# Kernel optimization log

Measured on AMD Instinct MI355X. Metric: run time of the kernel, lower is better.

The kernel has to match this reference:

```python
import jax, jax.numpy as jnp
import numpy as np

EPS = 1e-5

def _act_quant(x, bits=8):
    # per-token absmax quantization to signed int range, dequantized (STE)
    qb = float(2 ** (bits - 1) - 1)  # 127 for 8 bits
    scale = qb / jnp.clip(jnp.max(jnp.abs(x), axis=-1, keepdims=True), EPS, None)
    x_dq = jnp.clip(jnp.round(x * scale), -qb, qb) / scale
    return x + jax.lax.stop_gradient(x_dq - x)

def _weight_quant(w):
    # BitNet b1.58 ternary weights: scale = mean |W|, values in {-1,0,1} * scale (STE)
    s = jnp.clip(jnp.mean(jnp.abs(w)), EPS, None)
    w_dq = jnp.clip(jnp.round(w / s), -1.0, 1.0) * s
    return w + jax.lax.stop_gradient(w_dq - w)

def _bitlinear(x, w, bits=8):
    # x: [..., in], w: [out, in]
    return jnp.einsum('bsi,oi->bso', _act_quant(x, bits), _weight_quant(w))

def setup_inputs() -> dict:
    key = jax.random.key(0)
    k1, k2, k3 = jax.random.split(key, 3)
    B, S, H = 4, 4096, 2048
    I = int(H * 2.0)
    return {
        'hidden_states': jax.random.normal(k1, (B, S, H), dtype=jnp.float32),
        'w_up': jax.random.normal(k2, (I, H), dtype=jnp.float32) * (1.0 / np.sqrt(H)),
        'w_down': jax.random.normal(k3, (H, I), dtype=jnp.float32) * (1.0 / np.sqrt(I)),
    }

def reference(hidden_states, w_up, w_down):
    bits = 8
    h = _bitlinear(hidden_states, w_up, bits)          # [B,S,I]
    h = jnp.square(jax.nn.relu(h))                      # squared ReLU
    # dropout p=0.0 (eval) -> identity
    out = _bitlinear(h, w_down, bits)                   # [B,S,H]
    return out
```

## Files before the change

### kernel.cpp

```cpp
#include <hip/hip_runtime.h>
#include <hip/hip_bf16.h>

typedef unsigned short u16;
typedef signed char i8_t;
typedef _Float16 half_t;
typedef float v4fl __attribute__((ext_vector_type(4)));
typedef _Float16 v8h __attribute__((ext_vector_type(8)));
typedef int v4i __attribute__((ext_vector_type(4)));
typedef signed char v8c __attribute__((ext_vector_type(8)));
typedef signed char v16c __attribute__((ext_vector_type(16)));

#define BM 128
#define BN 128
#define BK 64

__device__ __forceinline__ float ternqf(float w, float s) {
    float q = rintf(w / s);
    return fminf(1.f, fmaxf(-1.f, q));
}

__device__ __forceinline__ void gload16(const void* g, void* l) {
    __builtin_amdgcn_global_load_lds(
        (const __attribute__((address_space(1))) void*)g,
        (__attribute__((address_space(3))) void*)l, 16, 0, 0);
}

__global__ void abssum_partial(const float* __restrict__ w, long n,
                               float* __restrict__ partial) {
    long i0 = ((long)blockIdx.x * 256 + threadIdx.x) * 8;
    long stride = (long)gridDim.x * 256 * 8;
    float s = 0.f;
    for (long i = i0; i < n; i += stride) {
        v4fl a = *(const v4fl*)(w + i);
        v4fl b = *(const v4fl*)(w + i + 4);
#pragma unroll
        for (int j = 0; j < 4; ++j) s += fabsf(a[j]) + fabsf(b[j]);
    }
#pragma unroll
    for (int off = 32; off > 0; off >>= 1) s += __shfl_down(s, off, 64);
    __shared__ __align__(16) float red[4];
    if ((threadIdx.x & 63) == 0) red[threadIdx.x >> 6] = s;
    __syncthreads();
    if (threadIdx.x == 0)
        partial[blockIdx.x] = (red[0] + red[1]) + (red[2] + red[3]);
}

__global__ void abssum_final(const float* __restrict__ part_up,
                             const float* __restrict__ part_dn,
                             float* __restrict__ scales, float inv) {
    const int wv = threadIdx.x >> 6;
    const int l = threadIdx.x & 63;
    const float* part = wv ? part_dn : part_up;
    float s = ((part[l] + part[l + 64]) + (part[l + 128] + part[l + 192]));
#pragma unroll
    for (int off = 32; off > 0; off >>= 1) s += __shfl_down(s, off, 64);
    if (l == 0) scales[wv] = fmaxf(s * inv, 1e-5f);
}

__global__ void wquant_kernel(const float* __restrict__ w, i8_t* __restrict__ wq,
                              const float* __restrict__ scale) {
    float s = scale[0];
    long i = ((long)blockIdx.x * 256 + threadIdx.x) * 8;
    v4fl a = *(const v4fl*)(w + i);
    v4fl b = *(const v4fl*)(w + i + 4);
    v8c o;
#pragma unroll
    for (int j = 0; j < 4; ++j) {
        o[j]     = (i8_t)(int)ternqf(a[j], s);
        o[j + 4] = (i8_t)(int)ternqf(b[j], s);
    }
    *(v8c*)(wq + i) = o;
}

__global__ void aquant_kernel(const float* __restrict__ src, i8_t* __restrict__ dst,
                              float* __restrict__ scale_out) {
    const int row = blockIdx.x;
    const int tid = threadIdx.x;
    const float* p = src + (size_t)row * 2048;
    float v[8];
    {
        v4fl a = *(const v4fl*)(p + tid * 8);
        v4fl b = *(const v4fl*)(p + tid * 8 + 4);
#pragma unroll
        for (int j = 0; j < 4; ++j) { v[j] = a[j]; v[j + 4] = b[j]; }
    }
    float amax = 0.f;
#pragma unroll
    for (int j = 0; j < 8; ++j) amax = fmaxf(amax, fabsf(v[j]));
#pragma unroll
    for (int off = 32; off > 0; off >>= 1) amax = fmaxf(amax, __shfl_xor(amax, off, 64));
    __shared__ __align__(16) float red[4];
    __shared__ float bsc;
    if ((tid & 63) == 0) red[tid >> 6] = amax;
    __syncthreads();
    if (tid == 0) {
        float m = fmaxf(fmaxf(red[0], red[1]), fmaxf(red[2], red[3]));
        m = fmaxf(m, 1e-5f);
        scale_out[row] = m / 127.f;
        bsc = 127.f / m;
    }
    __syncthreads();
    float sc = bsc;
    v8c o;
#pragma unroll
    for (int j = 0; j < 8; ++j) {
        float t = rintf(v[j] * sc);
        o[j] = (i8_t)(int)fminf(127.f, fmaxf(-127.f, t));
    }
    *(v8c*)(dst + (size_t)row * 2048 + tid * 8) = o;
}

template <int NV>
__global__ void hquant_kernel(const float* __restrict__ h, i8_t* __restrict__ hq,
                              float* __restrict__ scale_out) {
    const int row = blockIdx.x;
    const int tid = threadIdx.x;
    const int W = NV * 2048;
    const float* p = h + (size_t)row * W + tid * (NV * 8);
    float v[NV * 8];
#pragma unroll
    for (int it = 0; it < NV * 2; ++it) {
        v4fl a = *(const v4fl*)(p + it * 4);
#pragma unroll
        for (int j = 0; j < 4; ++j) v[it * 4 + j] = a[j];
    }
    float amax = 0.f;
#pragma unroll
    for (int j = 0; j < NV * 8; ++j) amax = fmaxf(amax, fabsf(v[j]));
#pragma unroll
    for (int off = 32; off > 0; off >>= 1) amax = fmaxf(amax, __shfl_xor(amax, off, 64));
    __shared__ __align__(16) float red[4];
    __shared__ float bsc;
    if ((tid & 63) == 0) red[tid >> 6] = amax;
    __syncthreads();
    if (tid == 0) {
        float m = fmaxf(fmaxf(red[0], red[1]), fmaxf(red[2], red[3]));
        m = fmaxf(m, 1e-5f);
        scale_out[row] = m / 127.f;
        bsc = 127.f / m;
    }
    __syncthreads();
    const float sc = bsc;
    i8_t* dst = hq + (size_t)row * W + tid * (NV * 8);
    v16c o;
#pragma unroll
    for (int j = 0; j < NV * 8; ++j) {
        float t = rintf(v[j] * sc);
        o[j] = (i8_t)(int)fminf(127.f, fmaxf(-127.f, t));
    }
    *(v16c*)dst = o;
}

template <typename T, int NV>
__global__ void hamax_kernel(const T* __restrict__ h, float* __restrict__ scale_out,
                             float* __restrict__ recip_out) {
    const int row = blockIdx.x;
    const int tid = threadIdx.x;
    const T* p = h + (size_t)row * (NV * 2048);
    float amax = 0.f;
#pragma unroll
    for (int it = 0; it < NV; ++it) {
        const T* s = p + ((size_t)it * 256 + tid) * 8;
#pragma unroll
        for (int j = 0; j < 8; ++j) amax = fmaxf(amax, fabsf((float)s[j]));
    }
#pragma unroll
    for (int off = 32; off > 0; off >>= 1) amax = fmaxf(amax, __shfl_xor(amax, off, 64));
    __shared__ __align__(16) float red[4];
    if ((tid & 63) == 0) red[tid >> 6] = amax;
    __syncthreads();
    if (tid == 0) {
        float m = fmaxf(fmaxf(red[0], red[1]), fmaxf(red[2], red[3]));
        m = fmaxf(m, 1e-5f);
        scale_out[row] = m / 127.f;
        recip_out[row] = 127.f / m;
    }
}

template <int ASRC, int EPI>
__launch_bounds__(256, 2)
__global__ void gemm_bt(const void* __restrict__ Av, const i8_t* __restrict__ B,
                        void* __restrict__ Cv,
                        const float* __restrict__ rowscale,
                        const float* __restrict__ arecip,
                        const float* __restrict__ wscale,
                        int M, int N, int K) {
    __shared__ __align__(16) i8_t As[BM * BK];
    __shared__ __align__(16) i8_t Bs[BN * BK];

    const int tid = threadIdx.x;

    const int gx = gridDim.x;
    const int nwg = gx * gridDim.y;
    int flat = blockIdx.y * gx + blockIdx.x;
    if ((nwg & 7) == 0) flat = (flat & 7) * (nwg >> 3) + (flat >> 3);
    const int n0 = (flat % gx) * BN;
    const int m0 = (flat / gx) * BM;

    const int srow = tid >> 2;
    const int scol = (tid & 3) * 16;
    const i8_t* gB0 = B + (size_t)(n0 + srow) * K + scol;
    const i8_t* gB1 = B + (size_t)(n0 + 64 + srow) * K + scol;
    i8_t* lB0 = Bs + tid * 16;
    i8_t* lB1 = Bs + 4096 + tid * 16;

    const i8_t* gA0 = nullptr;
    const i8_t* gA1 = nullptr;
    i8_t* lA0 = As + tid * 16;
    i8_t* lA1 = As + 4096 + tid * 16;
    if (ASRC == 0) {
        gA0 = (const i8_t*)Av + (size_t)(m0 + srow) * K + scol;
        gA1 = (const i8_t*)Av + (size_t)(m0 + 64 + srow) * K + scol;
    }

    const int qrow = tid >> 1;
    const int qcol = (tid & 1) * 32;
    const float* gA32 = (const float*)Av + (size_t)(m0 + qrow) * K + qcol;
    const half_t* gAh = (const half_t*)Av + (size_t)(m0 + qrow) * K + qcol;
    i8_t* qdst = As + qrow * BK + qcol;
    const float qsc = (ASRC != 0) ? arecip[m0 + qrow] : 0.f;

    const int w = tid >> 6, l = tid & 63;
    const int wr = w >> 1, wc = w & 1;
    const int lrow = l & 15, lq = l >> 4;

    v4i acc[4][4];
#pragma unroll
    for (int a = 0; a < 4; ++a)
#pragma unroll
        for (int b = 0; b < 4; ++b) acc[a][b] = (v4i){0, 0, 0, 0};

    const int kiters = K / BK;
    for (int kt = 0; kt < kiters; ++kt) {
        const int off = kt * BK;
        v16c r0, r1;
        if (ASRC == 1) {
#pragma unroll
            for (int c = 0; c < 4; ++c) {
                v4fl f0 = *(const v4fl*)(gA32 + off + c * 4);
                v4fl f1 = *(const v4fl*)(gA32 + off + 16 + c * 4);
#pragma unroll
                for (int e = 0; e < 4; ++e) {
                    float t0 = rintf(f0[e] * qsc);
                    float t1 = rintf(f1[e] * qsc);
                    r0[c * 4 + e] = (i8_t)(int)fminf(127.f, fmaxf(-127.f, t0));
                    r1[c * 4 + e] = (i8_t)(int)fminf(127.f, fmaxf(-127.f, t1));
                }
            }
        } else if (ASRC == 2) {
#pragma unroll
            for (int c = 0; c < 2; ++c) {
                v8h h0 = *(const v8h*)(gAh + off + c * 8);
                v8h h1 = *(const v8h*)(gAh + off + 16 + c * 8);
#pragma unroll
                for (int e = 0; e < 8; ++e) {
                    float t0 = rintf((float)h0[e] * qsc);
                    float t1 = rintf((float)h1[e] * qsc);
                    r0[c * 8 + e] = (i8_t)(int)fminf(127.f, fmaxf(-127.f, t0));
                    r1[c * 8 + e] = (i8_t)(int)fminf(127.f, fmaxf(-127.f, t1));
                }
            }
        }
        __syncthreads();
        gload16(gB0 + off, lB0);
        gload16(gB1 + off, lB1);
        if (ASRC == 0) {
            gload16(gA0 + off, lA0);
            gload16(gA1 + off, lA1);
        } else {
            *(v16c*)qdst = r0;
            *(v16c*)(qdst + 16) = r1;
        }
        __syncthreads();

        v4i af[4], bfr[4];
#pragma unroll
        for (int mi = 0; mi < 4; ++mi)
            af[mi] = *(const v4i*)(As + (wr * 64 + mi * 16 + lrow) * BK + lq * 16);
#pragma unroll
        for (int nj = 0; nj < 4; ++nj)
            bfr[nj] = *(const v4i*)(Bs + (wc * 64 + nj * 16 + lrow) * BK + lq * 16);
#pragma unroll
        for (int mi = 0; mi < 4; ++mi)
#pragma unroll
            for (int nj = 0; nj < 4; ++nj)
                acc[mi][nj] = __builtin_amdgcn_mfma_i32_16x16x64_i8(
                    af[mi], bfr[nj], acc[mi][nj], 0, 0, 0);
    }

    const float sw = wscale[0];
#pragma unroll
    for (int mi = 0; mi < 4; ++mi) {
#pragma unroll
        for (int r = 0; r < 4; ++r) {
            const int row = m0 + wr * 64 + mi * 16 + lq * 4 + r;
            const float rs = sw * rowscale[row];
#pragma unroll
            for (int nj = 0; nj < 4; ++nj) {
                const int col = n0 + wc * 64 + nj * 16 + lrow;
                float v = (float)acc[mi][nj][r] * rs;
                if (EPI == 0) {
                    ((float*)Cv)[(size_t)row * N + col] = v;
                } else if (EPI == 1) {
                    v = fmaxf(v, 0.f); v = v * v;
                    ((half_t*)Cv)[(size_t)row * N + col] = (half_t)v;
                } else {
                    v = fmaxf(v, 0.f); v = v * v;
                    ((float*)Cv)[(size_t)row * N + col] = v;
                }
            }
        }
    }
}

extern "C" void kernel_launch(void* const* d_in, const int* in_sizes, int n_in,
                              void* d_out, int out_size, void* d_ws, size_t ws_size,
                              hipStream_t stream) {
    const float* x   = (const float*)d_in[0];
    const float* wup = (const float*)d_in[1];
    const float* wdn = (const float*)d_in[2];

    const int H = 2048;
    const int T = in_sizes[0] / H;
    const int I = in_sizes[1] / H;
    const long nw = (long)in_sizes[1];
    const float winv = 1.0f / (float)nw;

    char* p = (char*)d_ws;
    float* scales  = (float*)p;
    float* part_up = (float*)(p + 256);
    float* part_dn = (float*)(p + 1280);
    float* a_scale = (float*)(p + 2304);
    float* h_scale = a_scale + T;
    float* h_recip = h_scale + T;
    size_t off = 2304 + (size_t)12 * T;
    off = (off + 255) & ~(size_t)255;
    i8_t* xq  = (i8_t*)(p + off); off += (size_t)T * H;
    off = (off + 255) & ~(size_t)255;
    i8_t* wqu = (i8_t*)(p + off); off += (size_t)I * H;
    off = (off + 255) & ~(size_t)255;
    i8_t* wqd = (i8_t*)(p + off); off += (size_t)H * I;
    off = (off + 255) & ~(size_t)255;
    void* h  = (void*)(p + off);
    i8_t* hq = (i8_t*)(p + off + (size_t)T * I * 4);

    const size_t need_full = off + (size_t)T * I * 5;
    const size_t need_h32  = off + (size_t)T * I * 4;
    const int mode = (ws_size == 0 || need_full <= ws_size) ? 0
                   : (need_h32 <= ws_size ? 1 : 2);

    abssum_partial<<<256, 256, 0, stream>>>(wup, nw, part_up);
    abssum_partial<<<256, 256, 0, stream>>>(wdn, nw, part_dn);
    abssum_final<<<1, 128, 0, stream>>>(part_up, part_dn, scales, winv);

    int wblocks = (int)(nw / 2048);
    wquant_kernel<<<wblocks, 256, 0, stream>>>(wup, wqu, scales + 0);
    wquant_kernel<<<wblocks, 256, 0, stream>>>(wdn, wqd, scales + 1);

    aquant_kernel<<<T, 256, 0, stream>>>(x, xq, a_scale);

    if (mode == 0) {
        gemm_bt<0, 2><<<dim3(I / BN, T / BM), 256, 0, stream>>>(
            xq, wqu, h, a_scale, nullptr, scales + 0, T, I, H);
        hquant_kernel<2><<<T, 256, 0, stream>>>((const float*)h, hq, h_scale);
        gemm_bt<0, 0><<<dim3(H / BN, T / BM), 256, 0, stream>>>(
            hq, wqd, d_out, h_scale, nullptr, scales + 1, T, H, I);
    } else if (mode == 1) {
        gemm_bt<0, 2><<<dim3(I / BN, T / BM), 256, 0, stream>>>(
            xq, wqu, h, a_scale, nullptr, scales + 0, T, I, H);
        hamax_kernel<float, 2><<<T, 256, 0, stream>>>((const float*)h, h_scale, h_recip);
        gemm_bt<1, 0><<<dim3(H / BN, T / BM), 256, 0, stream>>>(
            h, wqd, d_out, h_scale, h_recip, scales + 1, T, H, I);
    } else {
        gemm_bt<0, 1><<<dim3(I / BN, T / BM), 256, 0, stream>>>(
            xq, wqu, h, a_scale, nullptr, scales + 0, T, I, H);
        hamax_kernel<half_t, 2><<<T, 256, 0, stream>>>((const half_t*)h, h_scale, h_recip);
        gemm_bt<2, 0><<<dim3(H / BN, T / BM), 256, 0, stream>>>(
            h, wqd, d_out, h_scale, h_recip, scales + 1, T, H, I);
    }
}
```

Before: 677.3 us.

## Add 256x256 int8 GEMM with swizzled LDS double buffering and async prefetch

Result: faster. 628.8 us (-7.2%).

```diff
diff --git a/kernel.cpp b/kernel.cpp
--- a/kernel.cpp
+++ b/kernel.cpp
@@ -1,7 +1,6 @@
 #include <hip/hip_runtime.h>
 #include <hip/hip_bf16.h>
 
-typedef unsigned short u16;
 typedef signed char i8_t;
 typedef _Float16 half_t;
 typedef float v4fl __attribute__((ext_vector_type(4)));
@@ -9,10 +8,6 @@
 typedef int v4i __attribute__((ext_vector_type(4)));
 typedef signed char v8c __attribute__((ext_vector_type(8)));
 typedef signed char v16c __attribute__((ext_vector_type(16)));
-
-#define BM 128
-#define BN 128
-#define BK 64
 
 __device__ __forceinline__ float ternqf(float w, float s) {
     float q = rintf(w / s);
@@ -177,6 +172,167 @@
     }
 }
 
+__device__ __forceinline__ void stage_tile256(const i8_t* __restrict__ g, int K,
+                                              i8_t* l, int tid) {
+#pragma unroll
+    for (int i = 0; i < 4; ++i) {
+        const int c = i * 512 + tid;
+        const int r = c >> 3;
+        const int lc = (((c & 7) ^ (r & 7)) << 4);
+        gload16(g + (size_t)r * K + lc, l + c * 16);
+    }
+}
+
+#define MIDBAR() do { \
+    __builtin_amdgcn_s_barrier(); \
+    __builtin_amdgcn_sched_barrier(0); \
+    asm volatile("s_waitcnt lgkmcnt(0)" ::: "memory"); \
+    __builtin_amdgcn_sched_barrier(0); } while (0)
+
+#define ENDBAR() do { \
+    __builtin_amdgcn_sched_barrier(0); \
+    __builtin_amdgcn_s_barrier(); \
+    __builtin_amdgcn_sched_barrier(0); } while (0)
+
+template <int EPI>
+__launch_bounds__(512, 2)
+__global__ void gemm_bt8(const i8_t* __restrict__ A, const i8_t* __restrict__ B,
+                         void* __restrict__ Cv,
+                         const float* __restrict__ rowscale,
+                         const float* __restrict__ wscale,
+                         int M, int N, int K) {
+    __shared__ __align__(16) i8_t smem[131072];
+
+    const int tid = threadIdx.x;
+
+    const int gx = gridDim.x;
+    const int nwg = gx * gridDim.y;
+    int flat = blockIdx.y * gx + blockIdx.x;
+    if ((nwg & 7) == 0) flat = (flat & 7) * (nwg >> 3) + (flat >> 3);
+    const int n0 = (flat % gx) * 256;
+    const int m0 = (flat / gx) * 256;
+
+    const i8_t* gA = A + (size_t)m0 * K;
+    const i8_t* gB = B + (size_t)n0 * K;
+
+    const int w = tid >> 6, l = tid & 63;
+    const int wr = w >> 2, wc = w & 3;
+    const int lrow = l & 15, lq = l >> 4;
+    const int swz = (lrow & 7) << 4;
+    const int c0 = (lq << 4) ^ swz;
+    const int aoff0 = ((wr * 128 + lrow) << 7) + c0;
+    const int boff0 = ((wc * 64 + lrow) << 7) + c0;
+
+    v4i acc[8][4];
+#pragma unroll
+    for (int a = 0; a < 8; ++a)
+#pragma unroll
+        for (int b = 0; b < 4; ++b) acc[a][b] = (v4i){0, 0, 0, 0};
+
+    const int NT = K >> 7;
+    stage_tile256(gB, K, smem + 32768, tid);
+    stage_tile256(gA, K, smem, tid);
+    stage_tile256(gB + 128, K, smem + 65536 + 32768, tid);
+    stage_tile256(gA + 128, K, smem + 65536, tid);
+    asm volatile("s_waitcnt vmcnt(8)" ::: "memory");
+    __builtin_amdgcn_s_barrier();
+    __builtin_amdgcn_sched_barrier(0);
+
+    for (int t = 0; t < NT; ++t) {
+        i8_t* Ab = smem + ((t & 1) << 16);
+        i8_t* Bb = Ab + 32768;
+        const bool pf = (t + 2 < NT);
+
+        v4i af[8], bf[4][2];
+#pragma unroll
+        for (int nj = 0; nj < 4; ++nj) {
+            bf[nj][0] = *(const v4i*)(Bb + (boff0 + (nj << 11)));
+            bf[nj][1] = *(const v4i*)(Bb + ((boff0 + (nj << 11)) ^ 64));
+        }
+#pragma unroll
+        for (int mi = 0; mi < 8; ++mi)
+            af[mi] = *(const v4i*)(Ab + (aoff0 + (mi << 11)));
+        MIDBAR();
+        __builtin_amdgcn_s_setprio(1);
+#pragma unroll
+        for (int mi = 0; mi < 8; ++mi)
+#pragma unroll
+            for (int nj = 0; nj < 2; ++nj)
+                acc[mi][nj] = __builtin_amdgcn_mfma_i32_16x16x64_i8(
+                    af[mi], bf[nj][0], acc[mi][nj], 0, 0, 0);
+        __builtin_amdgcn_s_setprio(0);
+        ENDBAR();
+
+        if (pf) stage_tile256(gB + (size_t)(t + 2) * 128, K, Bb, tid);
+        MIDBAR();
+        __builtin_amdgcn_s_setprio(1);
+#pragma unroll
+        for (int mi = 0; mi < 8; ++mi)
+#pragma unroll
+            for (int nj = 2; nj < 4; ++nj)
+                acc[mi][nj] = __builtin_amdgcn_mfma_i32_16x16x64_i8(
+                    af[mi], bf[nj][0], acc[mi][nj], 0, 0, 0);
+        __builtin_amdgcn_s_setprio(0);
+        ENDBAR();
+
+#pragma unroll
+        for (int mi = 0; mi < 8; ++mi)
+            af[mi] = *(const v4i*)(Ab + ((aoff0 + (mi << 11)) ^ 64));
+        MIDBAR();
+        __builtin_amdgcn_s_setprio(1);
+#pragma unroll
+        for (int mi = 0; mi < 8; ++mi)
+#pragma unroll
+            for (int nj = 0; nj < 2; ++nj)
+                acc[mi][nj] = __builtin_amdgcn_mfma_i32_16x16x64_i8(
+                    af[mi], bf[nj][1], acc[mi][nj], 0, 0, 0);
+        __builtin_amdgcn_s_setprio(0);
+        ENDBAR();
+
+        if (pf) stage_tile256(gA + (size_t)(t + 2) * 128, K, Ab, tid);
+        MIDBAR();
+        __builtin_amdgcn_s_setprio(1);
+#pragma unroll
+        for (int mi = 0; mi < 8; ++mi)
+#pragma unroll
+            for (int nj = 2; nj < 4; ++nj)
+                acc[mi][nj] = __builtin_amdgcn_mfma_i32_16x16x64_i8(
+                    af[mi], bf[nj][1], acc[mi][nj], 0, 0, 0);
+        __builtin_amdgcn_s_setprio(0);
+        __builtin_amdgcn_sched_barrier(0);
+        if (pf) {
+            asm volatile("s_waitcnt vmcnt(8)" ::: "memory");
+        } else if (t + 1 < NT) {
+            asm volatile("s_waitcnt vmcnt(0)" ::: "memory");
+        }
+        if (t + 1 < NT) {
+            __builtin_amdgcn_s_barrier();
+            __builtin_amdgcn_sched_barrier(0);
+        }
+    }
+
+    const float sw = wscale[0];
+#pragma unroll
+    for (int mi = 0; mi < 8; ++mi) {
+#pragma unroll
+        for (int r = 0; r < 4; ++r) {
+            const int row = m0 + wr * 128 + mi * 16 + lq * 4 + r;
+            const float rs = sw * rowscale[row];
+#pragma unroll
+            for (int nj = 0; nj < 4; ++nj) {
+                const int col = n0 + wc * 64 + nj * 16 + lrow;
+                float v = (float)acc[mi][nj][r] * rs;
+                if (EPI == 0) {
+                    ((float*)Cv)[(size_t)row * N + col] = v;
+                } else {
+                    v = fmaxf(v, 0.f); v = v * v;
+                    ((float*)Cv)[(size_t)row * N + col] = v;
+                }
+            }
+        }
+    }
+}
+
 template <int ASRC, int EPI>
 __launch_bounds__(256, 2)
 __global__ void gemm_bt(const void* __restrict__ Av, const i8_t* __restrict__ B,
@@ -185,17 +341,16 @@
                         const float* __restrict__ arecip,
                         const float* __restrict__ wscale,
                         int M, int N, int K) {
-    __shared__ __align__(16) i8_t As[BM * BK];
-    __shared__ __align__(16) i8_t Bs[BN * BK];
+    __shared__ __align__(16) i8_t As[128 * 64];
+    __shared__ __align__(16) i8_t Bs[128 * 64];
 
     const int tid = threadIdx.x;
-
     const int gx = gridDim.x;
     const int nwg = gx * gridDim.y;
     int flat = blockIdx.y * gx + blockIdx.x;
     if ((nwg & 7) == 0) flat = (flat & 7) * (nwg >> 3) + (flat >> 3);
-    const int n0 = (flat % gx) * BN;
-    const int m0 = (flat / gx) * BM;
+    const int n0 = (flat % gx) * 128;
+    const int m0 = (flat / gx) * 128;
 
     const int srow = tid >> 2;
     const int scol = (tid & 3) * 16;
@@ -217,7 +372,7 @@
     const int qcol = (tid & 1) * 32;
     const float* gA32 = (const float*)Av + (size_t)(m0 + qrow) * K + qcol;
     const half_t* gAh = (const half_t*)Av + (size_t)(m0 + qrow) * K + qcol;
-    i8_t* qdst = As + qrow * BK + qcol;
+    i8_t* qdst = As + qrow * 64 + qcol;
     const float qsc = (ASRC != 0) ? arecip[m0 + qrow] : 0.f;
 
     const int w = tid >> 6, l = tid & 63;
@@ -230,9 +385,9 @@
 #pragma unroll
         for (int b = 0; b < 4; ++b) acc[a][b] = (v4i){0, 0, 0, 0};
 
-    const int kiters = K / BK;
+    const int kiters = K / 64;
     for (int kt = 0; kt < kiters; ++kt) {
-        const int off = kt * BK;
+        const int off = kt * 64;
         v16c r0, r1;
         if (ASRC == 1) {
 #pragma unroll
@@ -276,10 +431,10 @@
         v4i af[4], bfr[4];
 #pragma unroll
         for (int mi = 0; mi < 4; ++mi)
-            af[mi] = *(const v4i*)(As + (wr * 64 + mi * 16 + lrow) * BK + lq * 16);
+            af[mi] = *(const v4i*)(As + (wr * 64 + mi * 16 + lrow) * 64 + lq * 16);
 #pragma unroll
         for (int nj = 0; nj < 4; ++nj)
-            bfr[nj] = *(const v4i*)(Bs + (wc * 64 + nj * 16 + lrow) * BK + lq * 16);
+            bfr[nj] = *(const v4i*)(Bs + (wc * 64 + nj * 16 + lrow) * 64 + lq * 16);
 #pragma unroll
         for (int mi = 0; mi < 4; ++mi)
 #pragma unroll
@@ -348,6 +503,8 @@
     const size_t need_h32  = off + (size_t)T * I * 4;
     const int mode = (ws_size == 0 || need_full <= ws_size) ? 0
                    : (need_h32 <= ws_size ? 1 : 2);
+    const bool big_ok = (T % 256 == 0) && (I % 256 == 0) && (H % 256 == 0) &&
+                        (H >= 256) && (I >= 256);
 
     abssum_partial<<<256, 256, 0, stream>>>(wup, nw, part_up);
     abssum_partial<<<256, 256, 0, stream>>>(wdn, nw, part_dn);
@@ -359,23 +516,29 @@
 
     aquant_kernel<<<T, 256, 0, stream>>>(x, xq, a_scale);
 
-    if (mode == 0) {
-        gemm_bt<0, 2><<<dim3(I / BN, T / BM), 256, 0, stream>>>(
+    if (mode == 0 && big_ok) {
+        gemm_bt8<2><<<dim3(I / 256, T / 256), 512, 0, stream>>>(
+            xq, wqu, h, a_scale, scales + 0, T, I, H);
+        hquant_kernel<2><<<T, 256, 0, stream>>>((const float*)h, hq, h_scale);
+        gemm_bt8<0><<<dim3(H / 256, T / 256), 512, 0, stream>>>(
+            hq, wqd, d_out, h_scale, scales + 1, T, H, I);
+    } else if (mode == 0) {
+        gemm_bt<0, 2><<<dim3(I / 128, T / 128), 256, 0, stream>>>(
             xq, wqu, h, a_scale, nullptr, scales + 0, T, I, H);
         hquant_kernel<2><<<T, 256, 0, stream>>>((const float*)h, hq, h_scale);
-        gemm_bt<0, 0><<<dim3(H / BN, T / BM), 256, 0, stream>>>(
+        gemm_bt<0, 0><<<dim3(H / 128, T / 128), 256, 0, stream>>>(
             hq, wqd, d_out, h_scale, nullptr, scales + 1, T, H, I);
     } else if (mode == 1) {
-        gemm_bt<0, 2><<<dim3(I / BN, T / BM), 256, 0, stream>>>(
+        gemm_bt<0, 2><<<dim3(I / 128, T / 128), 256, 0, stream>>>(
             xq, wqu, h, a_scale, nullptr, scales + 0, T, I, H);
         hamax_kernel<float, 2><<<T, 256, 0, stream>>>((const float*)h, h_scale, h_recip);
-        gemm_bt<1, 0><<<dim3(H / BN, T / BM), 256, 0, stream>>>(
+        gemm_bt<1, 0><<<dim3(H / 128, T / 128), 256, 0, stream>>>(
             h, wqd, d_out, h_scale, h_recip, scales + 1, T, H, I);
     } else {
-        gemm_bt<0, 1><<<dim3(I / BN, T / BM), 256, 0, stream>>>(
+        gemm_bt<0, 1><<<dim3(I / 128, T / 128), 256, 0, stream>>>(
             xq, wqu, h, a_scale, nullptr, scales + 0, T, I, H);
         hamax_kernel<half_t, 2><<<T, 256, 0, stream>>>((const half_t*)h, h_scale, h_recip);
-        gemm_bt<2, 0><<<dim3(H / BN, T / BM), 256, 0, stream>>>(
+        gemm_bt<2, 0><<<dim3(H / 128, T / 128), 256, 0, stream>>>(
             h, wqd, d_out, h_scale, h_recip, scales + 1, T, H, I);
     }
 }
```
